# Kernel optimization log

Hardware: AMD Instinct MI355X
Metric: run time of the kernel (lower is better)

Reference implementation:

```python
import jax, jax.numpy as jnp
import numpy as np

BATCH, CHANNEL, LENGTH, CHI, D = 1024, 10, 784, 64, 2


def _dims():
    # dims[n+1] = min(d**(n+1), chi, d**(length-n-1)); dims[0] = 1
    dims = [1]
    for n in range(LENGTH):
        dims.append(min(D ** (n + 1), CHI, D ** (LENGTH - n - 1)))
    return dims


def _site_mask():
    # zero out tensor entries outside the [dims[n], dims[n+1]] bond block; this is
    # exactly equivalent to the per-site slicing in the torch code, but lets us
    # run one uniform lax.scan over sites with full-chi tensors.
    dims = _dims()
    mask = np.zeros((LENGTH, CHI, 1, CHI), np.float32)
    for n in range(LENGTH):
        mask[n, :dims[n], :, :dims[n + 1]] = 1.0
    return jnp.asarray(mask)


def setup_inputs() -> dict:
    key = jax.random.key(0)
    k1, k2 = jax.random.split(key)
    x = jax.random.uniform(k1, (BATCH, D, LENGTH), dtype=jnp.float32)
    scale = 1.0 / np.sqrt(CHI * D)
    tensors = jax.random.normal(k2, (CHANNEL, LENGTH, CHI, D, CHI), dtype=jnp.float32) * scale
    return {"x": x, "tensors": tensors}


def _forward(x, tensors):
    # mask == slicing tensors[:, nt, :dims[nt], :, :dims[nt+1]] at every site
    mt = tensors * _site_mask()[None]              # (c, L, chi, d, chi)
    A = jnp.transpose(mt, (1, 0, 2, 3, 4))         # (L, c, chi, d, chi)
    xs = jnp.transpose(x, (2, 0, 1))               # (L, n, d)
    is_last = jnp.arange(LENGTH) == LENGTH - 1
    y0 = jnp.zeros((x.shape[0], CHANNEL, CHI), x.dtype).at[:, :, 0].set(1.0)

    def step(y, inp):
        a, xv, last = inp
        y = jnp.einsum('nca,caib,ni->ncb', y, a, xv)
        # activation '(tanh(y)+1)/2' on all sites except the last one
        y = jnp.where(last, y, (jnp.tanh(y) + 1.0) * 0.5)
        return y, None

    y, _ = jax.lax.scan(step, y0, (A, xs, is_last))
    return y[:, :, :1]  # dims[length] == 1 -> (n, channel, 1)


def reference(x, tensors):
    return _forward(x, tensors)
```

## Files before the change

### kernel.cpp

```cpp
#include <hip/hip_runtime.h>
#include <hip/hip_bf16.h>


#define LEN 784
#define NCH 10

typedef short bf16x8 __attribute__((ext_vector_type(8)));
typedef float f32x4  __attribute__((ext_vector_type(4)));
typedef unsigned int u32x4 __attribute__((ext_vector_type(4)));

#define WSA_SHORTS ((size_t)NCH * LEN * 8192)
#define WSX_FLOATS ((size_t)1024 * 2 * LEN)
#define WS_NEED (WSA_SHORTS * 2 + WSX_FLOATS * 4)

#define XSCALE -2.88539008177792681f
#define XUNDO  -0.34657359027997264f

static __device__ __forceinline__ unsigned short f2bf(float f) {
    union { __hip_bfloat16 h; unsigned short s; } u;
    u.h = __float2bfloat16(f);
    return u.s;
}

static __device__ __forceinline__ unsigned pack_bf2(float a, float b) {
    union { __hip_bfloat162 h; unsigned u; } c;
    c.h = __float22bfloat162_rn(float2{a, b});
    return c.u;
}

static __device__ __forceinline__ int site_dlim(int m) {
    int e1 = m < 6 ? (1 << m) : 64;
    int e2 = (LEN - m) < 6 ? (1 << (LEN - m)) : 64;
    return e1 < e2 ? e1 : e2;
}

__global__ __launch_bounds__(1024) void prepass(const float* __restrict__ x,
                                                const float* __restrict__ tens,
                                                short* __restrict__ wsA,
                                                float* __restrict__ wsX)
{
    const int bid = blockIdx.x;
    const int t = threadIdx.x;
    if (bid < NCH * LEN) {
        const int site = bid % LEN;
        const int dlim = site_dlim(site);
        const int mt = t >> 8, ii = (t >> 7) & 1, kf = (t >> 6) & 1, l = t & 63;
        const int l15 = l & 15;
        const int bout = 32 * (mt >> 1) + 8 * (l15 >> 2) + 4 * (mt & 1) + (l15 & 3);
        const int a0 = 32 * kf + 8 * (l >> 4);
        const float* src = tens + (size_t)bid * 8192;
        unsigned int wv[4];
        #pragma unroll
        for (int p = 0; p < 4; ++p) {
            int aA = a0 + 2 * p, aB = a0 + 2 * p + 1;
            float f0 = (aA < dlim) ? src[(size_t)aA * 128 + ii * 64 + bout] : 0.f;
            float f1 = (aB < dlim) ? src[(size_t)aB * 128 + ii * 64 + bout] : 0.f;
            wv[p] = (unsigned)f2bf(f0) | ((unsigned)f2bf(f1) << 16);
        }
        *(int4*)(wsA + (size_t)bid * 8192 + (size_t)t * 8) = *(int4*)wv;
    } else {
        int b = bid - NCH * LEN;
        if (t < LEN) {
            float v0 = x[(size_t)b * (2 * LEN) + t] * XSCALE;
            float v1 = x[(size_t)b * (2 * LEN) + LEN + t] * XSCALE;
            float2 pk; pk.x = v0; pk.y = v1;
            *(float2*)(wsX + (size_t)b * (2 * LEN) + 2 * t) = pk;
        }
    }
}

#define GLOAD(dst, voffr, sbase, imm) \
    asm volatile("global_load_dwordx4 %0, %1, %2 offset:" #imm \
                 : "=v"(dst) : "v"(voffr), "s"(sbase))

#define WAIT16() do { \
    asm volatile("s_waitcnt vmcnt(16)" ::: "memory"); \
    __builtin_amdgcn_sched_barrier(0); \
} while (0)

__global__ __launch_bounds__(64) void mps_fwd13(const short* __restrict__ wsA,
                                                const float* __restrict__ wsX,
                                                float* __restrict__ out)
{
    const int lane = threadIdx.x;
    const int g = lane >> 4, l15 = lane & 15;

    const int p = blockIdx.x;
    const int gidx = (p & 7) * 80 + (p >> 3);
    const int ch = gidx >> 6;
    const int b0 = (gidx & 63) * 16;

    const short* asrc = wsA + (size_t)ch * LEN * 8192;
    const float* xsrc = wsX + (size_t)(b0 + l15) * (2 * LEN);

    const int voff0 = lane * 16;
    const int voff1 = voff0 + 4096;
    const int voff2 = voff0 + 8192;
    const int voff3 = voff0 + 12288;

    const f32x4 Z = (f32x4){0.f, 0.f, 0.f, 0.f};

    bf16x8 tf0, tf1;
    #pragma unroll
    for (int j = 0; j < 8; ++j) { tf0[j] = 0; tf1[j] = 0; }
    if (g == 0) tf0[0] = (short)0x3F80;

    auto loadA = [&](int site, u32x4 (&A)[16]) {
        site = site < LEN ? site : LEN - 1;
        const short* sb = asrc + (size_t)site * 8192;
        GLOAD(A[0],  voff0, sb, 0);    GLOAD(A[1],  voff0, sb, 1024);
        GLOAD(A[2],  voff0, sb, 2048); GLOAD(A[3],  voff0, sb, 3072);
        GLOAD(A[4],  voff1, sb, 0);    GLOAD(A[5],  voff1, sb, 1024);
        GLOAD(A[6],  voff1, sb, 2048); GLOAD(A[7],  voff1, sb, 3072);
        GLOAD(A[8],  voff2, sb, 0);    GLOAD(A[9],  voff2, sb, 1024);
        GLOAD(A[10], voff2, sb, 2048); GLOAD(A[11], voff2, sb, 3072);
        GLOAD(A[12], voff3, sb, 0);    GLOAD(A[13], voff3, sb, 1024);
        GLOAD(A[14], voff3, sb, 2048); GLOAD(A[15], voff3, sb, 3072);
    };

    auto loadX = [&](int nb, float4& qa, float4& qb) {
        nb = nb <= LEN - 4 ? nb : LEN - 4;
        const float* sx = xsrc + 2 * nb;
        asm volatile("global_load_dwordx4 %0, %1, off"
                     : "=v"(qa) : "v"(sx));
        asm volatile("global_load_dwordx4 %0, %1, off offset:16"
                     : "=v"(qb) : "v"(sx));
    };

    auto body = [&](int n, u32x4 (&Ac)[16], u32x4 (&Al)[16],
                    float x0s, float x1s) {
        loadA(n + 2, Al);
        __builtin_amdgcn_sched_barrier(0);

        f32x4 acc[4][2];
        __builtin_amdgcn_s_setprio(1);
        #pragma unroll
        for (int mt = 0; mt < 4; ++mt)
            #pragma unroll
            for (int ii = 0; ii < 2; ++ii) {
                f32x4 a0 = __builtin_amdgcn_mfma_f32_16x16x32_bf16(
                    __builtin_bit_cast(bf16x8, Ac[mt * 4 + ii * 2 + 0]),
                    tf0, Z, 0, 0, 0);
                acc[mt][ii] = __builtin_amdgcn_mfma_f32_16x16x32_bf16(
                    __builtin_bit_cast(bf16x8, Ac[mt * 4 + ii * 2 + 1]),
                    tf1, a0, 0, 0, 0);
            }
        __builtin_amdgcn_s_setprio(0);

        if (n == LEN - 1) {
            if (g == 0) {
                float v = (x0s * acc[0][0][0] + x1s * acc[0][1][0]) * XUNDO;
                out[(size_t)(b0 + l15) * NCH + ch] = v;
            }
        } else {
            unsigned pk[8];
            #pragma unroll
            for (int mt = 0; mt < 4; ++mt) {
                float s[4];
                #pragma unroll
                for (int r = 0; r < 4; ++r) {
                    float u = x0s * acc[mt][0][r] + x1s * acc[mt][1][r];
                    float ex = __builtin_amdgcn_exp2f(u);
                    s[r] = __builtin_amdgcn_rcpf(1.0f + ex);
                }
                pk[mt * 2 + 0] = pack_bf2(s[0], s[1]);
                pk[mt * 2 + 1] = pack_bf2(s[2], s[3]);
            }
            union { unsigned u[4]; bf16x8 v; } u0, u1;
            u0.u[0] = pk[0]; u0.u[1] = pk[1]; u0.u[2] = pk[2]; u0.u[3] = pk[3];
            u1.u[0] = pk[4]; u1.u[1] = pk[5]; u1.u[2] = pk[6]; u1.u[3] = pk[7];
            tf0 = u0.v; tf1 = u1.v;
        }

        WAIT16();
    };

    u32x4 B0[16], B1[16], B2[16], B3[16];
    float4 xa, xb, xna, xnb;

    loadX(0, xa, xb);
    loadA(0, B0);
    loadA(1, B1);
    WAIT16();

    for (int nb = 0; nb < LEN; nb += 4) {
        loadX(nb + 4, xna, xnb);
        body(nb + 0, B0, B2, xa.x, xa.y);
        body(nb + 1, B1, B3, xa.z, xa.w);
        body(nb + 2, B2, B0, xb.x, xb.y);
        body(nb + 3, B3, B1, xb.z, xb.w);
        xa = xna; xb = xnb;
    }
}

__global__ __launch_bounds__(64) void mps_fwd13_fb(const float* __restrict__ x,
                                                   const float* __restrict__ tens,
                                                   float* __restrict__ out)
{
    const int lane = threadIdx.x;
    const int g = lane >> 4, l15 = lane & 15;
    const int p = blockIdx.x;
    const int gidx = (p & 7) * 80 + (p >> 3);
    const int ch = gidx >> 6;
    const int b0 = (gidx & 63) * 16;

    const float* tsrc = tens + (size_t)ch * LEN * 8192;
    const float* xsrc = x + (size_t)(b0 + l15) * (2 * LEN);

    bf16x8 tf0, tf1;
    #pragma unroll
    for (int j = 0; j < 8; ++j) { tf0[j] = 0; tf1[j] = 0; }
    if (g == 0) tf0[0] = (short)0x3F80;

    for (int n = 0; n < LEN; ++n) {
        const int dlim = site_dlim(n);
        const float* sb = tsrc + (size_t)n * 8192;
        bf16x8 A[16];
        #pragma unroll
        for (int f = 0; f < 16; ++f) {
            int mt = f >> 2, ii = (f >> 1) & 1, kf = f & 1;
            int bout = 32 * (mt >> 1) + 8 * (l15 >> 2) + 4 * (mt & 1) + (l15 & 3);
            int a0 = 32 * kf + 8 * g;
            unsigned int wv[4];
            #pragma unroll
            for (int q2 = 0; q2 < 4; ++q2) {
                int aA = a0 + 2 * q2, aB = aA + 1;
                float f0 = (aA < dlim) ? sb[(size_t)aA * 128 + ii * 64 + bout] : 0.f;
                float f1 = (aB < dlim) ? sb[(size_t)aB * 128 + ii * 64 + bout] : 0.f;
                wv[q2] = (unsigned)f2bf(f0) | ((unsigned)f2bf(f1) << 16);
            }
            A[f] = *(bf16x8*)wv;
        }
        float x0s = xsrc[n] * XSCALE, x1s = xsrc[LEN + n] * XSCALE;

        f32x4 acc[4][2];
        #pragma unroll
        for (int mt = 0; mt < 4; ++mt)
            #pragma unroll
            for (int ii = 0; ii < 2; ++ii)
                acc[mt][ii] = (f32x4){0.f, 0.f, 0.f, 0.f};
        #pragma unroll
        for (int kf = 0; kf < 2; ++kf) {
            bf16x8 tfk = kf ? tf1 : tf0;
            #pragma unroll
            for (int mt = 0; mt < 4; ++mt)
                #pragma unroll
                for (int ii = 0; ii < 2; ++ii)
                    acc[mt][ii] = __builtin_amdgcn_mfma_f32_16x16x32_bf16(
                        A[mt * 4 + ii * 2 + kf], tfk, acc[mt][ii], 0, 0, 0);
        }

        if (n == LEN - 1) {
            if (g == 0) {
                float v = (x0s * acc[0][0][0] + x1s * acc[0][1][0]) * XUNDO;
                out[(size_t)(b0 + l15) * NCH + ch] = v;
            }
        } else {
            unsigned pk[8];
            #pragma unroll
            for (int mt = 0; mt < 4; ++mt)
                #pragma unroll
                for (int rp = 0; rp < 2; ++rp) {
                    unsigned short sv[2];
                    #pragma unroll
                    for (int q2 = 0; q2 < 2; ++q2) {
                        int r = 2 * rp + q2;
                        float u = x0s * acc[mt][0][r] + x1s * acc[mt][1][r];
                        float sg = __builtin_amdgcn_rcpf(1.0f + exp2f(u));
                        sv[q2] = f2bf(sg);
                    }
                    pk[mt * 2 + rp] = (unsigned)sv[0] | ((unsigned)sv[1] << 16);
                }
            union { unsigned u[4]; bf16x8 v; } u0, u1;
            u0.u[0] = pk[0]; u0.u[1] = pk[1]; u0.u[2] = pk[2]; u0.u[3] = pk[3];
            u1.u[0] = pk[4]; u1.u[1] = pk[5]; u1.u[2] = pk[6]; u1.u[3] = pk[7];
            tf0 = u0.v; tf1 = u1.v;
        }
    }
}

extern "C" void kernel_launch(void* const* d_in, const int* in_sizes, int n_in,
                              void* d_out, int out_size, void* d_ws, size_t ws_size,
                              hipStream_t stream) {
    (void)in_sizes; (void)n_in; (void)out_size;
    const float* x    = (const float*)d_in[0];
    const float* tens = (const float*)d_in[1];
    float* out = (float*)d_out;
    if (ws_size >= WS_NEED) {
        short* wsA = (short*)d_ws;
        float* wsX = (float*)((char*)d_ws + WSA_SHORTS * 2);
        hipLaunchKernelGGL(prepass, dim3(NCH * LEN + 1024), dim3(1024), 0, stream,
                           x, tens, wsA, wsX);
        hipLaunchKernelGGL(mps_fwd13, dim3(640), dim3(64), 0, stream,
                           wsA, wsX, out);
    } else {
        hipLaunchKernelGGL(mps_fwd13_fb, dim3(640), dim3(64), 0, stream,
                           x, tens, out);
    }
}
```

Before: 514.5 us.

## Split each batch tile's MPS recurrence across two wavefronts with LDS exchange

```diff
diff --git a/kernel.cpp b/kernel.cpp
--- a/kernel.cpp
+++ b/kernel.cpp
@@ -44,10 +44,12 @@
     if (bid < NCH * LEN) {
         const int site = bid % LEN;
         const int dlim = site_dlim(site);
-        const int mt = t >> 8, ii = (t >> 7) & 1, kf = (t >> 6) & 1, l = t & 63;
-        const int l15 = l & 15;
-        const int bout = 32 * (mt >> 1) + 8 * (l15 >> 2) + 4 * (mt & 1) + (l15 & 3);
-        const int a0 = 32 * kf + 8 * (l >> 4);
+        const int w = t >> 9, mt = (t >> 8) & 1, ii = (t >> 7) & 1,
+                  kfp = (t >> 6) & 1, l = t & 63;
+        const int g = l >> 4, l15 = l & 15;
+        const int kf = kfp ^ w;
+        const int bout = 32 * w + 8 * (l15 >> 2) + 4 * mt + (l15 & 3);
+        const int a0 = 32 * kf + 8 * g;
         const float* src = tens + (size_t)bid * 8192;
         unsigned int wv[4];
         #pragma unroll
@@ -73,16 +75,22 @@
     asm volatile("global_load_dwordx4 %0, %1, %2 offset:" #imm \
                  : "=v"(dst) : "v"(voffr), "s"(sbase))
 
-#define WAIT16() do { \
-    asm volatile("s_waitcnt vmcnt(16)" ::: "memory"); \
+#define WAIT8() do { \
+    asm volatile("s_waitcnt vmcnt(8)" ::: "memory"); \
     __builtin_amdgcn_sched_barrier(0); \
 } while (0)
 
-__global__ __launch_bounds__(64) void mps_fwd13(const short* __restrict__ wsA,
-                                                const float* __restrict__ wsX,
-                                                float* __restrict__ out)
+#define BARX() asm volatile("s_waitcnt lgkmcnt(0)\n\ts_barrier" ::: "memory")
+
+__global__ __launch_bounds__(128) void mps_fwd15(const short* __restrict__ wsA,
+                                                 const float* __restrict__ wsX,
+                                                 float* __restrict__ out)
 {
-    const int lane = threadIdx.x;
+    __shared__ short ex[2][2][512];
+
+    const int tid = threadIdx.x;
+    const int lane = tid & 63;
+    const int w = tid >> 6;
     const int g = lane >> 4, l15 = lane & 15;
 
     const int p = blockIdx.x;
@@ -93,29 +101,23 @@
     const short* asrc = wsA + (size_t)ch * LEN * 8192;
     const float* xsrc = wsX + (size_t)(b0 + l15) * (2 * LEN);
 
-    const int voff0 = lane * 16;
+    const int voff0 = w * 8192 + lane * 16;
     const int voff1 = voff0 + 4096;
-    const int voff2 = voff0 + 8192;
-    const int voff3 = voff0 + 12288;
 
     const f32x4 Z = (f32x4){0.f, 0.f, 0.f, 0.f};
 
-    bf16x8 tf0, tf1;
+    bf16x8 tf_self;
     #pragma unroll
-    for (int j = 0; j < 8; ++j) { tf0[j] = 0; tf1[j] = 0; }
-    if (g == 0) tf0[0] = (short)0x3F80;
-
-    auto loadA = [&](int site, u32x4 (&A)[16]) {
+    for (int j = 0; j < 8; ++j) tf_self[j] = 0;
+    if (w == 0 && g == 0) tf_self[0] = (short)0x3F80;
+
+    auto loadA = [&](int site, u32x4 (&A)[8]) {
         site = site < LEN ? site : LEN - 1;
         const short* sb = asrc + (size_t)site * 8192;
-        GLOAD(A[0],  voff0, sb, 0);    GLOAD(A[1],  voff0, sb, 1024);
-        GLOAD(A[2],  voff0, sb, 2048); GLOAD(A[3],  voff0, sb, 3072);
-        GLOAD(A[4],  voff1, sb, 0);    GLOAD(A[5],  voff1, sb, 1024);
-        GLOAD(A[6],  voff1, sb, 2048); GLOAD(A[7],  voff1, sb, 3072);
-        GLOAD(A[8],  voff2, sb, 0);    GLOAD(A[9],  voff2, sb, 1024);
-        GLOAD(A[10], voff2, sb, 2048); GLOAD(A[11], voff2, sb, 3072);
-        GLOAD(A[12], voff3, sb, 0);    GLOAD(A[13], voff3, sb, 1024);
-        GLOAD(A[14], voff3, sb, 2048); GLOAD(A[15], voff3, sb, 3072);
+        GLOAD(A[0], voff0, sb, 0);    GLOAD(A[1], voff0, sb, 1024);
+        GLOAD(A[2], voff0, sb, 2048); GLOAD(A[3], voff0, sb, 3072);
+        GLOAD(A[4], voff1, sb, 0);    GLOAD(A[5], voff1, sb, 1024);
+        GLOAD(A[6], voff1, sb, 2048); GLOAD(A[7], voff1, sb, 3072);
     };
 
     auto loadX = [&](int nb, float4& qa, float4& qb) {
@@ -127,61 +129,69 @@
                      : "=v"(qb) : "v"(sx));
     };
 
-    auto body = [&](int n, u32x4 (&Ac)[16], u32x4 (&Al)[16],
+    auto body = [&](int n, u32x4 (&Ac)[8], u32x4 (&Al)[8],
                     float x0s, float x1s) {
         loadA(n + 2, Al);
         __builtin_amdgcn_sched_barrier(0);
 
-        f32x4 acc[4][2];
+        bf16x8 tfo = *(const bf16x8*)&ex[n & 1][1 - w][lane * 8];
+
+        f32x4 acc[2][2];
         __builtin_amdgcn_s_setprio(1);
         #pragma unroll
-        for (int mt = 0; mt < 4; ++mt)
-            #pragma unroll
-            for (int ii = 0; ii < 2; ++ii) {
-                f32x4 a0 = __builtin_amdgcn_mfma_f32_16x16x32_bf16(
+        for (int mt = 0; mt < 2; ++mt)
+            #pragma unroll
+            for (int ii = 0; ii < 2; ++ii)
+                acc[mt][ii] = __builtin_amdgcn_mfma_f32_16x16x32_bf16(
                     __builtin_bit_cast(bf16x8, Ac[mt * 4 + ii * 2 + 0]),
-                    tf0, Z, 0, 0, 0);
+                    tf_self, Z, 0, 0, 0);
+        #pragma unroll
+        for (int mt = 0; mt < 2; ++mt)
+            #pragma unroll
+            for (int ii = 0; ii < 2; ++ii)
                 acc[mt][ii] = __builtin_amdgcn_mfma_f32_16x16x32_bf16(
                     __builtin_bit_cast(bf16x8, Ac[mt * 4 + ii * 2 + 1]),
-                    tf1, a0, 0, 0, 0);
-            }
+                    tfo, acc[mt][ii], 0, 0, 0);
         __builtin_amdgcn_s_setprio(0);
 
         if (n == LEN - 1) {
-            if (g == 0) {
+            if (w == 0 && g == 0) {
                 float v = (x0s * acc[0][0][0] + x1s * acc[0][1][0]) * XUNDO;
                 out[(size_t)(b0 + l15) * NCH + ch] = v;
             }
         } else {
-            unsigned pk[8];
-            #pragma unroll
-            for (int mt = 0; mt < 4; ++mt) {
+            unsigned pk[4];
+            #pragma unroll
+            for (int mt = 0; mt < 2; ++mt) {
                 float s[4];
                 #pragma unroll
                 for (int r = 0; r < 4; ++r) {
                     float u = x0s * acc[mt][0][r] + x1s * acc[mt][1][r];
-                    float ex = __builtin_amdgcn_exp2f(u);
-                    s[r] = __builtin_amdgcn_rcpf(1.0f + ex);
+                    float exv = __builtin_amdgcn_exp2f(u);
+                    s[r] = __builtin_amdgcn_rcpf(1.0f + exv);
                 }
                 pk[mt * 2 + 0] = pack_bf2(s[0], s[1]);
                 pk[mt * 2 + 1] = pack_bf2(s[2], s[3]);
             }
-            union { unsigned u[4]; bf16x8 v; } u0, u1;
-            u0.u[0] = pk[0]; u0.u[1] = pk[1]; u0.u[2] = pk[2]; u0.u[3] = pk[3];
-            u1.u[0] = pk[4]; u1.u[1] = pk[5]; u1.u[2] = pk[6]; u1.u[3] = pk[7];
-            tf0 = u0.v; tf1 = u1.v;
-        }
-
-        WAIT16();
+            union { unsigned u[4]; bf16x8 v; } nf;
+            nf.u[0] = pk[0]; nf.u[1] = pk[1]; nf.u[2] = pk[2]; nf.u[3] = pk[3];
+            tf_self = nf.v;
+            *(bf16x8*)&ex[(n + 1) & 1][w][lane * 8] = nf.v;
+        }
+
+        WAIT8();
+        BARX();
     };
 
-    u32x4 B0[16], B1[16], B2[16], B3[16];
+    u32x4 B0[8], B1[8], B2[8], B3[8];
     float4 xa, xb, xna, xnb;
 
+    *(bf16x8*)&ex[0][w][lane * 8] = tf_self;
     loadX(0, xa, xb);
     loadA(0, B0);
     loadA(1, B1);
-    WAIT16();
+    WAIT8();
+    BARX();
 
     for (int nb = 0; nb < LEN; nb += 4) {
         loadX(nb + 4, xna, xnb);
@@ -193,7 +203,7 @@
     }
 }
 
-__global__ __launch_bounds__(64) void mps_fwd13_fb(const float* __restrict__ x,
+__global__ __launch_bounds__(64) void mps_fwd15_fb(const float* __restrict__ x,
                                                    const float* __restrict__ tens,
                                                    float* __restrict__ out)
 {
@@ -291,10 +301,10 @@
         float* wsX = (float*)((char*)d_ws + WSA_SHORTS * 2);
         hipLaunchKernelGGL(prepass, dim3(NCH * LEN + 1024), dim3(1024), 0, stream,
                            x, tens, wsA, wsX);
-        hipLaunchKernelGGL(mps_fwd13, dim3(640), dim3(64), 0, stream,
+        hipLaunchKernelGGL(mps_fwd15, dim3(640), dim3(128), 0, stream,
                            wsA, wsX, out);
     } else {
-        hipLaunchKernelGGL(mps_fwd13_fb, dim3(640), dim3(64), 0, stream,
+        hipLaunchKernelGGL(mps_fwd15_fb, dim3(640), dim3(64), 0, stream,
                            x, tens, out);
     }
 }
```

New measurement: 528.2 us. 1.03x slower.
